# Optimization experiments

Hardware: AMD Instinct MI355X
Metric: run time of the kernel (lower is better)

Reference implementation:

```python
import jax, jax.numpy as jnp
import numpy as np

N, F, E, D, H, G = 65536, 256, 16, 256, 512, 256  # nodes, feat, experts(node_num), emb_dim, hidden_dim, graphs


def setup_inputs() -> dict:
    key = jax.random.key(0)
    ks = jax.random.split(key, 11)
    scale = 0.02
    return {
        "node_fea": jax.random.normal(ks[0], (N, F), jnp.float32),
        "masks": jax.random.uniform(ks[1], (N, F), jnp.float32),
        "node_type": jax.random.randint(ks[2], (N,), 0, E),
        "g_node_id": jnp.sort(jax.random.randint(ks[3], (G,), 0, N)),
        "label": jax.random.randint(ks[4], (G,), 0, 2),
        "W_emb": jax.random.normal(ks[5], (E, F, D), jnp.float32) * scale,
        "b_emb": jax.random.normal(ks[6], (E, D), jnp.float32) * scale,
        "W_hid": jax.random.normal(ks[7], (D, H), jnp.float32) * scale,
        "b_hid": jax.random.normal(ks[8], (H,), jnp.float32) * scale,
        "W_out": jax.random.normal(ks[9], (H, 2), jnp.float32) * scale,
        "b_out": jax.random.normal(ks[10], (2,), jnp.float32) * scale,
    }


def reference(node_fea, masks, node_type, g_node_id, label,
              W_emb, b_emb, W_hid, b_hid, W_out, b_out):
    # --- node_embedding: per-node type-routed linear (grouped GEMM form) ---
    xm = node_fea * masks                                   # [N, F]
    # run every expert densely, then select each node's expert output
    all_emb = jnp.einsum('nf,efd->ned', xm, W_emb) + b_emb[None]   # [N, E, D]
    emb = jnp.take_along_axis(all_emb, node_type[:, None, None], axis=1)[:, 0, :]  # [N, D]
    # --- hidden_fc (dropout in eval mode = identity) ---
    h = emb @ W_hid + b_hid                                 # [N, H]
    # --- pick first node of each batched graph ---
    g_emb = h[g_node_id]                                    # [G, H]
    # --- output layer: Linear + Softmax ---
    probs = jax.nn.softmax(g_emb @ W_out + b_out, axis=-1)  # [G, 2]
    # --- CrossEntropyLoss(reduction='sum') applied to probs (as in source) ---
    logp = jax.nn.log_softmax(probs, axis=-1)
    loss = -jnp.sum(jnp.take_along_axis(logp, label[:, None], axis=1))
    return probs, loss
```

## Files before the change

kernel.cpp:

```cpp
#include <hip/hip_runtime.h>
#include <math.h>

#define FF 256
#define EE 16
#define DD 256
#define HH 512
#define GG 256

__global__ __launch_bounds__(256) void fused_graph_kernel(
    const float* __restrict__ node_fea,
    const float* __restrict__ masks,
    const int*   __restrict__ node_type,
    const int*   __restrict__ g_node_id,
    const int*   __restrict__ label,
    const float* __restrict__ W_emb,
    const float* __restrict__ b_emb,
    const float* __restrict__ W_hid,
    const float* __restrict__ b_hid,
    const float* __restrict__ W_out,
    const float* __restrict__ b_out,
    float* __restrict__ probs_out,
    float* __restrict__ loss_ws)
{
    __shared__ __align__(16) float xm[FF];
    __shared__ __align__(16) float part[4][DD];
    __shared__ __align__(16) float emb[DD];
    __shared__ float red0[4];
    __shared__ float red1[4];

    const int g = blockIdx.x;
    const int t = threadIdx.x;
    const int w = t >> 6;
    const int l = t & 63;
    const int c = l << 2;
    const int n = g_node_id[g];
    const int e = node_type[n];

    {
        size_t base = (size_t)n * FF + t;
        xm[t] = node_fea[base] * masks[base];
    }
    __syncthreads();

    {
        const float* __restrict__ Wb = W_emb + (size_t)e * FF * DD;
        float4 acc = {0.f, 0.f, 0.f, 0.f};
        #pragma unroll 8
        for (int i = 0; i < 64; ++i) {
            const int f = (w << 6) + i;
            const float s = xm[f];
            const float4 wv = *(const float4*)(Wb + (size_t)f * DD + c);
            acc.x = fmaf(s, wv.x, acc.x);
            acc.y = fmaf(s, wv.y, acc.y);
            acc.z = fmaf(s, wv.z, acc.z);
            acc.w = fmaf(s, wv.w, acc.w);
        }
        *(float4*)&part[w][c] = acc;
    }
    __syncthreads();

    emb[t] = part[0][t] + part[1][t] + part[2][t] + part[3][t]
           + b_emb[e * DD + t];
    __syncthreads();

    float z0p, z1p;
    {
        float4 ha, hb;
        if (w == 0) {
            ha = *(const float4*)(b_hid + c);
            hb = *(const float4*)(b_hid + 256 + c);
        } else {
            ha = (float4){0.f, 0.f, 0.f, 0.f};
            hb = (float4){0.f, 0.f, 0.f, 0.f};
        }
        #pragma unroll 8
        for (int i = 0; i < 64; ++i) {
            const int d = (w << 6) + i;
            const float s = emb[d];
            const float4 wa = *(const float4*)(W_hid + (size_t)d * HH + c);
            const float4 wb = *(const float4*)(W_hid + (size_t)d * HH + c + 256);
            ha.x = fmaf(s, wa.x, ha.x);
            ha.y = fmaf(s, wa.y, ha.y);
            ha.z = fmaf(s, wa.z, ha.z);
            ha.w = fmaf(s, wa.w, ha.w);
            hb.x = fmaf(s, wb.x, hb.x);
            hb.y = fmaf(s, wb.y, hb.y);
            hb.z = fmaf(s, wb.z, hb.z);
            hb.w = fmaf(s, wb.w, hb.w);
        }
        const float4 o0a = *(const float4*)(W_out + 2 * c);
        const float4 o0b = *(const float4*)(W_out + 2 * c + 4);
        const float4 o1a = *(const float4*)(W_out + 2 * (c + 256));
        const float4 o1b = *(const float4*)(W_out + 2 * (c + 256) + 4);
        z0p = ha.x * o0a.x + ha.y * o0a.z + ha.z * o0b.x + ha.w * o0b.z
            + hb.x * o1a.x + hb.y * o1a.z + hb.z * o1b.x + hb.w * o1b.z;
        z1p = ha.x * o0a.y + ha.y * o0a.w + ha.z * o0b.y + ha.w * o0b.w
            + hb.x * o1a.y + hb.y * o1a.w + hb.z * o1b.y + hb.w * o1b.w;
    }

    for (int off = 32; off > 0; off >>= 1) {
        z0p += __shfl_down(z0p, off, 64);
        z1p += __shfl_down(z1p, off, 64);
    }
    if (l == 0) { red0[w] = z0p; red1[w] = z1p; }
    __syncthreads();

    if (t == 0) {
        float z0 = b_out[0] + red0[0] + red0[1] + red0[2] + red0[3];
        float z1 = b_out[1] + red1[0] + red1[1] + red1[2] + red1[3];
        float m  = fmaxf(z0, z1);
        float e0 = expf(z0 - m), e1 = expf(z1 - m);
        float inv = 1.0f / (e0 + e1);
        float p0 = e0 * inv, p1 = e1 * inv;
        probs_out[2 * g + 0] = p0;
        probs_out[2 * g + 1] = p1;
        float mp  = fmaxf(p0, p1);
        float lse = mp + logf(expf(p0 - mp) + expf(p1 - mp));
        float pl  = (label[g] == 0) ? p0 : p1;
        loss_ws[g] = lse - pl;
    }
}

__global__ __launch_bounds__(256) void loss_reduce_kernel(
    const float* __restrict__ loss_ws, float* __restrict__ out)
{
    __shared__ float red[4];
    int t = threadIdx.x;
    float v = loss_ws[t];
    for (int off = 32; off > 0; off >>= 1) v += __shfl_down(v, off, 64);
    if ((t & 63) == 0) red[t >> 6] = v;
    __syncthreads();
    if (t == 0) out[0] = red[0] + red[1] + red[2] + red[3];
}

extern "C" void kernel_launch(void* const* d_in, const int* in_sizes, int n_in,
                              void* d_out, int out_size, void* d_ws, size_t ws_size,
                              hipStream_t stream) {
    const float* node_fea  = (const float*)d_in[0];
    const float* masks     = (const float*)d_in[1];
    const int*   node_type = (const int*)  d_in[2];
    const int*   g_node_id = (const int*)  d_in[3];
    const int*   label     = (const int*)  d_in[4];
    const float* W_emb     = (const float*)d_in[5];
    const float* b_emb     = (const float*)d_in[6];
    const float* W_hid     = (const float*)d_in[7];
    const float* b_hid     = (const float*)d_in[8];
    const float* W_out     = (const float*)d_in[9];
    const float* b_out     = (const float*)d_in[10];

    float* out = (float*)d_out;
    float* ws  = (float*)d_ws;

    fused_graph_kernel<<<GG, 256, 0, stream>>>(
        node_fea, masks, node_type, g_node_id, label,
        W_emb, b_emb, W_hid, b_hid, W_out, b_out,
        out, ws);

    loss_reduce_kernel<<<1, 256, 0, stream>>>(ws, out + GG * 2);
}
```

Baseline: 149.3 us.

## Fold linear layers into per-expert 2-column weights before gathering graph nodes

Because the embedding, hidden and output layers are all linear, the weights are pre-multiplied each call (W_emb·W_hid·W_out per expert, plus the folded biases) into a 16x256x2 matrix. Each selected node then needs only a 256-long dot product against its expert's folded weights. The per-graph kernel is replaced by a single 1024-thread block that also does the loss reduction, which removes a separate launch. The fold re-reads all of W_emb and W_hid in 64 blocks, and changing the summation order changes floating-point rounding slightly.

```diff
diff --git a/kernel.cpp b/kernel.cpp
--- a/kernel.cpp
+++ b/kernel.cpp
@@ -1,136 +1,158 @@
 #include <hip/hip_runtime.h>
 #include <math.h>
 
+#define NN 65536
 #define FF 256
 #define EE 16
 #define DD 256
 #define HH 512
 #define GG 256
 
-__global__ __launch_bounds__(256) void fused_graph_kernel(
-    const float* __restrict__ node_fea,
-    const float* __restrict__ masks,
-    const int*   __restrict__ node_type,
-    const int*   __restrict__ g_node_id,
-    const int*   __restrict__ label,
+
+__global__ __launch_bounds__(256) void fold_kernel(
     const float* __restrict__ W_emb,
     const float* __restrict__ b_emb,
     const float* __restrict__ W_hid,
     const float* __restrict__ b_hid,
     const float* __restrict__ W_out,
     const float* __restrict__ b_out,
-    float* __restrict__ probs_out,
-    float* __restrict__ loss_ws)
+    float* __restrict__ fold,
+    float* __restrict__ bfold)
 {
-    __shared__ __align__(16) float xm[FF];
-    __shared__ __align__(16) float part[4][DD];
-    __shared__ __align__(16) float emb[DD];
-    __shared__ float red0[4];
-    __shared__ float red1[4];
+    __shared__ __align__(16) float wo[2 * HH];
+    __shared__ __align__(16) float wtmp[2 * DD];
 
-    const int g = blockIdx.x;
     const int t = threadIdx.x;
-    const int w = t >> 6;
-    const int l = t & 63;
-    const int c = l << 2;
-    const int n = g_node_id[g];
-    const int e = node_type[n];
+    const int e = blockIdx.x >> 2;
+    const int r = blockIdx.x & 3;
+
+    *(float4*)(wo + 4 * t) = *(const float4*)(W_out + 4 * t);
+    __syncthreads();
 
     {
-        size_t base = (size_t)n * FF + t;
-        xm[t] = node_fea[base] * masks[base];
+        const float* __restrict__ Wr = W_hid + (size_t)t * HH;
+        float a0 = 0.f, a1 = 0.f;
+        #pragma unroll 8
+        for (int i = 0; i < HH / 4; ++i) {
+            const float4 wh = *(const float4*)(Wr + 4 * i);
+            const float4 o0 = *(const float4*)(wo + 8 * i);
+            const float4 o1 = *(const float4*)(wo + 8 * i + 4);
+            a0 = fmaf(wh.x, o0.x, a0);  a1 = fmaf(wh.x, o0.y, a1);
+            a0 = fmaf(wh.y, o0.z, a0);  a1 = fmaf(wh.y, o0.w, a1);
+            a0 = fmaf(wh.z, o1.x, a0);  a1 = fmaf(wh.z, o1.y, a1);
+            a0 = fmaf(wh.w, o1.z, a0);  a1 = fmaf(wh.w, o1.w, a1);
+        }
+        wtmp[2 * t]     = a0;
+        wtmp[2 * t + 1] = a1;
     }
     __syncthreads();
 
     {
-        const float* __restrict__ Wb = W_emb + (size_t)e * FF * DD;
-        float4 acc = {0.f, 0.f, 0.f, 0.f};
-        #pragma unroll 8
-        for (int i = 0; i < 64; ++i) {
-            const int f = (w << 6) + i;
-            const float s = xm[f];
-            const float4 wv = *(const float4*)(Wb + (size_t)f * DD + c);
-            acc.x = fmaf(s, wv.x, acc.x);
-            acc.y = fmaf(s, wv.y, acc.y);
-            acc.z = fmaf(s, wv.z, acc.z);
-            acc.w = fmaf(s, wv.w, acc.w);
+        const int row = (r << 6) + (t >> 2);
+        const int d0  = (t & 3) << 6;
+        const float* __restrict__ We =
+            W_emb + ((size_t)e * FF + row) * DD + d0;
+        float z0 = 0.f, z1 = 0.f;
+        #pragma unroll 4
+        for (int i = 0; i < 16; ++i) {
+            const float4 wv = *(const float4*)(We + 4 * i);
+            const int d2 = 2 * (d0 + 4 * i);
+            z0 = fmaf(wv.x, wtmp[d2 + 0], z0);  z1 = fmaf(wv.x, wtmp[d2 + 1], z1);
+            z0 = fmaf(wv.y, wtmp[d2 + 2], z0);  z1 = fmaf(wv.y, wtmp[d2 + 3], z1);
+            z0 = fmaf(wv.z, wtmp[d2 + 4], z0);  z1 = fmaf(wv.z, wtmp[d2 + 5], z1);
+            z0 = fmaf(wv.w, wtmp[d2 + 6], z0);  z1 = fmaf(wv.w, wtmp[d2 + 7], z1);
         }
-        *(float4*)&part[w][c] = acc;
+        z0 += __shfl_xor(z0, 1, 64);  z1 += __shfl_xor(z1, 1, 64);
+        z0 += __shfl_xor(z0, 2, 64);  z1 += __shfl_xor(z1, 2, 64);
+        if ((t & 3) == 0)
+            *(float2*)(fold + ((size_t)e * FF + row) * 2) = (float2){z0, z1};
+    }
+
+    if (r == 0 && t < 64) {
+        float c0 = 0.f, c1 = 0.f;
+        const float4 bh0 = *(const float4*)(b_hid + 8 * t);
+        const float4 bh1 = *(const float4*)(b_hid + 8 * t + 4);
+        const int h2 = 16 * t;
+        c0 = fmaf(bh0.x, wo[h2 +  0], c0);  c1 = fmaf(bh0.x, wo[h2 +  1], c1);
+        c0 = fmaf(bh0.y, wo[h2 +  2], c0);  c1 = fmaf(bh0.y, wo[h2 +  3], c1);
+        c0 = fmaf(bh0.z, wo[h2 +  4], c0);  c1 = fmaf(bh0.z, wo[h2 +  5], c1);
+        c0 = fmaf(bh0.w, wo[h2 +  6], c0);  c1 = fmaf(bh0.w, wo[h2 +  7], c1);
+        c0 = fmaf(bh1.x, wo[h2 +  8], c0);  c1 = fmaf(bh1.x, wo[h2 +  9], c1);
+        c0 = fmaf(bh1.y, wo[h2 + 10], c0);  c1 = fmaf(bh1.y, wo[h2 + 11], c1);
+        c0 = fmaf(bh1.z, wo[h2 + 12], c0);  c1 = fmaf(bh1.z, wo[h2 + 13], c1);
+        c0 = fmaf(bh1.w, wo[h2 + 14], c0);  c1 = fmaf(bh1.w, wo[h2 + 15], c1);
+        const float4 be = *(const float4*)(b_emb + e * DD + 4 * t);
+        const int d2 = 8 * t;
+        c0 = fmaf(be.x, wtmp[d2 + 0], c0);  c1 = fmaf(be.x, wtmp[d2 + 1], c1);
+        c0 = fmaf(be.y, wtmp[d2 + 2], c0);  c1 = fmaf(be.y, wtmp[d2 + 3], c1);
+        c0 = fmaf(be.z, wtmp[d2 + 4], c0);  c1 = fmaf(be.z, wtmp[d2 + 5], c1);
+        c0 = fmaf(be.w, wtmp[d2 + 6], c0);  c1 = fmaf(be.w, wtmp[d2 + 7], c1);
+        for (int off = 32; off; off >>= 1) {
+            c0 += __shfl_down(c0, off, 64);
+            c1 += __shfl_down(c1, off, 64);
+        }
+        if (t == 0) {
+            bfold[2 * e + 0] = c0 + b_out[0];
+            bfold[2 * e + 1] = c1 + b_out[1];
+        }
+    }
+}
+
+__global__ __launch_bounds__(1024) void graph_loss_kernel(
+    const float* __restrict__ node_fea,
+    const float* __restrict__ masks,
+    const int*   __restrict__ node_type,
+    const int*   __restrict__ g_node_id,
+    const int*   __restrict__ label,
+    const float* __restrict__ fold,
+    const float* __restrict__ bfold,
+    float* __restrict__ out)
+{
+    __shared__ float lterm[GG];
+    const int t = threadIdx.x;
+    const int w = t >> 6;
+    const int l = t & 63;
+
+    #pragma unroll
+    for (int p = 0; p < GG / 16; ++p) {
+        const int g = (p << 4) + w;
+        const int n = g_node_id[g];
+        const int e = node_type[n];
+        const size_t nb = (size_t)n * FF + (l << 2);
+        const float4 x = *(const float4*)(node_fea + nb);
+        const float4 m = *(const float4*)(masks + nb);
+        const float* fr = fold + e * (FF * 2) + (l << 3);
+        const float4 wa = *(const float4*)(fr);
+        const float4 wb = *(const float4*)(fr + 4);
+        const float x0 = x.x * m.x, x1 = x.y * m.y;
+        const float x2 = x.z * m.z, x3 = x.w * m.w;
+        float z0 = x0 * wa.x + x1 * wa.z + x2 * wb.x + x3 * wb.z;
+        float z1 = x0 * wa.y + x1 * wa.w + x2 * wb.y + x3 * wb.w;
+        for (int off = 32; off; off >>= 1) {
+            z0 += __shfl_down(z0, off, 64);
+            z1 += __shfl_down(z1, off, 64);
+        }
+        if (l == 0) {
+            z0 += bfold[2 * e + 0];
+            z1 += bfold[2 * e + 1];
+            const float mz = fmaxf(z0, z1);
+            const float e0 = expf(z0 - mz), e1 = expf(z1 - mz);
+            const float inv = 1.0f / (e0 + e1);
+            const float p0 = e0 * inv, p1 = e1 * inv;
+            out[2 * g + 0] = p0;
+            out[2 * g + 1] = p1;
+            const float mp  = fmaxf(p0, p1);
+            const float lse = mp + logf(expf(p0 - mp) + expf(p1 - mp));
+            lterm[g] = lse - ((label[g] == 0) ? p0 : p1);
+        }
     }
     __syncthreads();
 
-    emb[t] = part[0][t] + part[1][t] + part[2][t] + part[3][t]
-           + b_emb[e * DD + t];
-    __syncthreads();
-
-    float z0p, z1p;
-    {
-        float4 ha, hb;
-        if (w == 0) {
-            ha = *(const float4*)(b_hid + c);
-            hb = *(const float4*)(b_hid + 256 + c);
-        } else {
-            ha = (float4){0.f, 0.f, 0.f, 0.f};
-            hb = (float4){0.f, 0.f, 0.f, 0.f};
-        }
-        #pragma unroll 8
-        for (int i = 0; i < 64; ++i) {
-            const int d = (w << 6) + i;
-            const float s = emb[d];
-            const float4 wa = *(const float4*)(W_hid + (size_t)d * HH + c);
-            const float4 wb = *(const float4*)(W_hid + (size_t)d * HH + c + 256);
-            ha.x = fmaf(s, wa.x, ha.x);
-            ha.y = fmaf(s, wa.y, ha.y);
-            ha.z = fmaf(s, wa.z, ha.z);
-            ha.w = fmaf(s, wa.w, ha.w);
-            hb.x = fmaf(s, wb.x, hb.x);
-            hb.y = fmaf(s, wb.y, hb.y);
-            hb.z = fmaf(s, wb.z, hb.z);
-            hb.w = fmaf(s, wb.w, hb.w);
-        }
-        const float4 o0a = *(const float4*)(W_out + 2 * c);
-        const float4 o0b = *(const float4*)(W_out + 2 * c + 4);
-        const float4 o1a = *(const float4*)(W_out + 2 * (c + 256));
-        const float4 o1b = *(const float4*)(W_out + 2 * (c + 256) + 4);
-        z0p = ha.x * o0a.x + ha.y * o0a.z + ha.z * o0b.x + ha.w * o0b.z
-            + hb.x * o1a.x + hb.y * o1a.z + hb.z * o1b.x + hb.w * o1b.z;
-        z1p = ha.x * o0a.y + ha.y * o0a.w + ha.z * o0b.y + ha.w * o0b.w
-            + hb.x * o1a.y + hb.y * o1a.w + hb.z * o1b.y + hb.w * o1b.w;
+    if (t < 64) {
+        float v = lterm[t] + lterm[t + 64] + lterm[t + 128] + lterm[t + 192];
+        for (int off = 32; off; off >>= 1) v += __shfl_down(v, off, 64);
+        if (t == 0) out[2 * GG] = v;
     }
-
-    for (int off = 32; off > 0; off >>= 1) {
-        z0p += __shfl_down(z0p, off, 64);
-        z1p += __shfl_down(z1p, off, 64);
-    }
-    if (l == 0) { red0[w] = z0p; red1[w] = z1p; }
-    __syncthreads();
-
-    if (t == 0) {
-        float z0 = b_out[0] + red0[0] + red0[1] + red0[2] + red0[3];
-        float z1 = b_out[1] + red1[0] + red1[1] + red1[2] + red1[3];
-        float m  = fmaxf(z0, z1);
-        float e0 = expf(z0 - m), e1 = expf(z1 - m);
-        float inv = 1.0f / (e0 + e1);
-        float p0 = e0 * inv, p1 = e1 * inv;
-        probs_out[2 * g + 0] = p0;
-        probs_out[2 * g + 1] = p1;
-        float mp  = fmaxf(p0, p1);
-        float lse = mp + logf(expf(p0 - mp) + expf(p1 - mp));
-        float pl  = (label[g] == 0) ? p0 : p1;
-        loss_ws[g] = lse - pl;
-    }
-}
-
-__global__ __launch_bounds__(256) void loss_reduce_kernel(
-    const float* __restrict__ loss_ws, float* __restrict__ out)
-{
-    __shared__ float red[4];
-    int t = threadIdx.x;
-    float v = loss_ws[t];
-    for (int off = 32; off > 0; off >>= 1) v += __shfl_down(v, off, 64);
-    if ((t & 63) == 0) red[t >> 6] = v;
-    __syncthreads();
-    if (t == 0) out[0] = red[0] + red[1] + red[2] + red[3];
 }
 
 extern "C" void kernel_launch(void* const* d_in, const int* in_sizes, int n_in,
@@ -148,13 +170,13 @@
     const float* W_out     = (const float*)d_in[9];
     const float* b_out     = (const float*)d_in[10];
 
-    float* out = (float*)d_out;
-    float* ws  = (float*)d_ws;
+    float* out   = (float*)d_out;
+    float* fold  = (float*)d_ws;
+    float* bfold = fold + EE * FF * 2;
 
-    fused_graph_kernel<<<GG, 256, 0, stream>>>(
-        node_fea, masks, node_type, g_node_id, label,
-        W_emb, b_emb, W_hid, b_hid, W_out, b_out,
-        out, ws);
+    fold_kernel<<<EE * 4, 256, 0, stream>>>(
+        W_emb, b_emb, W_hid, b_hid, W_out, b_out, fold, bfold);
 
-    loss_reduce_kernel<<<1, 256, 0, stream>>>(ws, out + GG * 2);
+    graph_loss_kernel<<<1, 1024, 0, stream>>>(
+        node_fea, masks, node_type, g_node_id, label, fold, bfold, out);
 }
```

After: 184.8 us. 1.24x slower.
